# Optimization experiments

Measured on AMD Instinct MI355X. Metric: run time of the kernel, lower is better.

Reference implementation:

```python
import jax, jax.numpy as jnp
import numpy as np

NQ, NT, NA = 10000, 50000, 50000
E_GR, E_LT, E_SIM, E_COMP, E_GEN = 50000, 50000, 80000, 100000, 50000
HID, NH, HC, DOT, NL = 512, 4, 128, 256, 2
NEG_SLOPE = 0.2  # PyG GATv2Conv default negative_slope


def _gatv2(x_src, x_dst, src, dst, Wl, bl, Wr, br, att, bias, n_dst):
    # GATv2: x_j = lin_l(x_src), x_i = lin_r(x_dst); e = att . leaky_relu(x_i + x_j)
    xl = (x_src @ Wl + bl).reshape(-1, NH, HC)   # [Ns,H,C]
    xr = (x_dst @ Wr + br).reshape(-1, NH, HC)   # [Nd,H,C]
    m = jax.nn.leaky_relu(xl[src] + xr[dst], NEG_SLOPE)      # [E,H,C]
    logits = jnp.einsum('ehc,hc->eh', m, att)                # [E,H]
    lmax = jax.lax.stop_gradient(jax.ops.segment_max(logits, dst, num_segments=n_dst))
    lmax = jnp.where(jnp.isfinite(lmax), lmax, 0.0)
    ex = jnp.exp(logits - lmax[dst])
    denom = jax.ops.segment_sum(ex, dst, num_segments=n_dst)
    alpha = ex / (denom[dst] + 1e-16)                        # softmax over incoming edges
    out = jax.ops.segment_sum(xl[src] * alpha[:, :, None], dst, num_segments=n_dst)
    return out.reshape(n_dst, NH * HC) + bias


def _layernorm(x, g, b):
    mu = x.mean(-1, keepdims=True)
    var = ((x - mu) ** 2).mean(-1, keepdims=True)
    return (x - mu) / jnp.sqrt(var + 1e-5) * g + b


def _forward(xq, xt, xa, answer_features,
             qp_W, qp_b, tp_W, tp_b, ap_W, ap_b,
             afp_W1, afp_b1, afp_W2, afp_b2,
             conv_Wl, conv_bl, conv_Wr, conv_br, conv_att, conv_bias,
             qh_W, qh_b, qh_g, qh_beta, rh_W, rh_b, rh_g, rh_beta, score_bias,
             ei_gr, ei_lt, ei_sim, ei_comp, ei_gen):
    hq = xq @ qp_W + qp_b
    ht = xt @ tp_W + tp_b
    ha = xa @ ap_W + ap_b
    # add_self_loops=True only for ('query','similar_to','query')
    loops = jnp.arange(NQ, dtype=ei_sim.dtype)
    sim_src = jnp.concatenate([ei_sim[0], loops])
    sim_dst = jnp.concatenate([ei_sim[1], loops])
    for l in range(NL):
        P = lambda r: (conv_Wl[l, r], conv_bl[l, r], conv_Wr[l, r], conv_br[l, r], conv_att[l, r], conv_bias[l, r])
        o_gr = _gatv2(hq, ht, ei_gr[0], ei_gr[1], *P(0), NT)          # query -> think
        o_rgr = _gatv2(ht, hq, ei_gr[1], ei_gr[0], *P(1), NQ)         # think -> query (rev)
        o_lt = _gatv2(ht, ha, ei_lt[0], ei_lt[1], *P(2), NA)          # think -> answer
        o_rlt = _gatv2(ha, ht, ei_lt[1], ei_lt[0], *P(3), NT)         # answer -> think (rev)
        o_sim = _gatv2(hq, hq, sim_src, sim_dst, *P(4), NQ)           # query -> query
        o_cmp = _gatv2(ht, ht, ei_comp[0], ei_comp[1], *P(5), NT)     # think -> think
        # HeteroConv aggr='mean' across relations per destination type, then relu
        hq = jax.nn.relu((o_rgr + o_sim) / 2.0)
        ht = jax.nn.relu((o_gr + o_rlt + o_cmp) / 3.0)
        ha = jax.nn.relu(o_lt)
    q_emb = hq[ei_gen[0]]
    a_emb = ha[ei_gen[1]]
    t_emb = ht[ei_gen[1]]  # faithful to source: think indexed with answer-side index
    af_emb = jax.nn.relu(answer_features @ afp_W1 + afp_b1) @ afp_W2 + afp_b2
    q = _layernorm(q_emb @ qh_W + qh_b, qh_g, qh_beta)
    r = _layernorm(jnp.concatenate([t_emb, a_emb, af_emb], -1) @ rh_W + rh_b, rh_g, rh_beta)
    return (q * r).sum(-1) / jnp.sqrt(jnp.float32(DOT)) + score_bias


def setup_inputs() -> dict:
    ks = jax.random.split(jax.random.key(0), 40)
    n = lambda j, shape, s=0.05: jax.random.normal(ks[j], shape, jnp.float32) * s
    ri = lambda j, shape, hi: jax.random.randint(ks[j], shape, 0, hi, jnp.int32)
    return dict(
        xq=n(0, (NQ, 384), 1.0), xt=n(1, (NT, 384), 1.0), xa=n(2, (NA, 384), 1.0),
        answer_features=n(3, (E_GEN, 6), 1.0),
        qp_W=n(4, (384, HID)), qp_b=n(5, (HID,)),
        tp_W=n(6, (384, HID)), tp_b=n(7, (HID,)),
        ap_W=n(8, (384, HID)), ap_b=n(9, (HID,)),
        afp_W1=n(10, (6, 64)), afp_b1=n(11, (64,)),
        afp_W2=n(12, (64, HID)), afp_b2=n(13, (HID,)),
        conv_Wl=n(14, (NL, 6, HID, HID)), conv_bl=n(15, (NL, 6, HID)),
        conv_Wr=n(16, (NL, 6, HID, HID)), conv_br=n(17, (NL, 6, HID)),
        conv_att=n(18, (NL, 6, NH, HC)), conv_bias=n(19, (NL, 6, HID)),
        qh_W=n(20, (HID, DOT)), qh_b=n(21, (DOT,)),
        qh_g=jnp.ones((DOT,), jnp.float32), qh_beta=jnp.zeros((DOT,), jnp.float32),
        rh_W=n(22, (HID * 3, DOT)), rh_b=n(23, (DOT,)),
        rh_g=jnp.ones((DOT,), jnp.float32), rh_beta=jnp.zeros((DOT,), jnp.float32),
        score_bias=jnp.zeros((1,), jnp.float32),
        ei_gr=jnp.stack([ri(24, (E_GR,), NQ), ri(25, (E_GR,), NT)]),
        ei_lt=jnp.stack([ri(26, (E_LT,), NT), ri(27, (E_LT,), NA)]),
        ei_sim=ri(28, (2, E_SIM), NQ),
        ei_comp=ri(29, (2, E_COMP), NT),
        ei_gen=jnp.stack([ri(30, (E_GEN,), NQ), ri(31, (E_GEN,), NA)]),
    )


def reference(xq, xt, xa, answer_features,
              qp_W, qp_b, tp_W, tp_b, ap_W, ap_b,
              afp_W1, afp_b1, afp_W2, afp_b2,
              conv_Wl, conv_bl, conv_Wr, conv_br, conv_att, conv_bias,
              qh_W, qh_b, qh_g, qh_beta, rh_W, rh_b, rh_g, rh_beta, score_bias,
              ei_gr, ei_lt, ei_sim, ei_comp, ei_gen):
    return _forward(xq, xt, xa, answer_features,
                    qp_W, qp_b, tp_W, tp_b, ap_W, ap_b,
                    afp_W1, afp_b1, afp_W2, afp_b2,
                    conv_Wl, conv_bl, conv_Wr, conv_br, conv_att, conv_bias,
                    qh_W, qh_b, qh_g, qh_beta, rh_W, rh_b, rh_g, rh_beta, score_bias,
                    ei_gr, ei_lt, ei_sim, ei_comp, ei_gen)
```

## Files before the change

kernel.cpp:

```cpp
#include <hip/hip_runtime.h>
#include <cstdio>
#include <type_traits>

#define NQ 10000
#define NT 50000
#define NA 50000
#define E_GR 50000
#define E_LT 50000
#define E_SIM 80000
#define E_COMP 100000
#define E_GEN 50000
#define NEG_SLOPE 0.2f

#define NDTOT 220000
#define NSTOT 220000
#define ETOT  390000
__device__ __constant__ const int c_degOff[7]  = {0, 50000, 60000, 110000, 120000, 170000, 220000};
__device__ __constant__ const int c_sOff[7]    = {0, 10000, 60000, 110000, 120000, 170000, 220000};
__device__ __constant__ const int c_eOff[7]    = {0, 50000, 100000, 150000, 240000, 340000, 390000};
__device__ __constant__ const int c_nb[6]      = {49, 10, 49, 10, 49, 49};
__device__ __constant__ const int c_nbOff[7]   = {0, 49, 59, 108, 118, 167, 216};
__device__ __constant__ const int c_snb[6]     = {10, 49, 49, 10, 49, 49};
__device__ __constant__ const int c_snbOff[7]  = {0, 10, 59, 108, 118, 167, 216};

typedef unsigned short bf16_t;
typedef unsigned int u32;
typedef __attribute__((ext_vector_type(8))) short short8v;
typedef __attribute__((ext_vector_type(4))) float f32x4;

__device__ __forceinline__ float bf2f(u32 bits) { return __uint_as_float(bits << 16); }
__device__ __forceinline__ u32 f2bf(float f) {
  u32 u = __float_as_uint(f);
  return (u + 0x7FFFu + ((u >> 16) & 1u)) >> 16;
}
__device__ __forceinline__ u32 pack2(float a, float b) { return f2bf(a) | (f2bf(b) << 16); }
__device__ __forceinline__ void unpack8(uint4 u, float* f) {
  f[0] = bf2f(u.x & 0xffffu); f[1] = bf2f(u.x >> 16);
  f[2] = bf2f(u.y & 0xffffu); f[3] = bf2f(u.y >> 16);
  f[4] = bf2f(u.z & 0xffffu); f[5] = bf2f(u.z >> 16);
  f[6] = bf2f(u.w & 0xffffu); f[7] = bf2f(u.w >> 16);
}

__device__ __forceinline__ void gload16(const void* g, void* l) {
  __builtin_amdgcn_global_load_lds(
      (const __attribute__((address_space(1))) void*)g,
      (__attribute__((address_space(3))) void*)l, 16, 0, 0);
}

struct GemmDesc {
  const bf16_t* A; const bf16_t* Bt; const float* bias; void* C;
  const int* ridx; int N; const int* Nc; int K;
};

template <typename CT>
__global__ __launch_bounds__(512, 4) void bgemm(
    GemmDesc d0, GemmDesc d1, GemmDesc d2, GemmDesc d3, int M, int accumulate)
{
  __shared__ short lds[3][12288];
  const int z = blockIdx.z;
  GemmDesc d = (z == 3) ? d3 : (z == 2) ? d2 : (z == 1) ? d1 : d0;
  int N = d.Nc ? *d.Nc : d.N;
  const int K = d.K;

  const int tid = threadIdx.x;
  const int ncol = gridDim.x;
  const int nband = (N + 127) >> 7;
  int lin = blockIdx.y * ncol + blockIdx.x;
  if (lin >= ncol * nband) return;

  int band, col;
  const int full = (nband >> 3) * 8 * ncol;
  if (lin < full) {
    int g = lin >> 3, x = lin & 7;
    band = x + 8 * (g / ncol);
    col  = g % ncol;
  } else {
    int r = lin - full;
    band = (nband & ~7) + r / ncol;
    col  = r % ncol;
  }
  const int bm = band * 128, bn = col * 256;

  const int lane = tid & 63;
  const int w = tid >> 6;
  const int wr = w >> 2, wc = w & 3;
  const int fr = lane & 15, fg = lane >> 4;

  const int kg = (((tid & 3) ^ ((tid >> 3) & 3)) << 3);
  const int rr = tid >> 2;
  int ra = min(bm + rr, N - 1);
  const bf16_t* gA0 = d.A + (size_t)(d.ridx ? d.ridx[ra] : ra) * K + kg;
  const bf16_t* gB0 = d.Bt + (size_t)(bn + rr) * K + kg;
  const bf16_t* gB1 = d.Bt + (size_t)(bn + 128 + rr) * K + kg;
  const int wb = w << 9;

  f32x4 acc[4][4];
#pragma unroll
  for (int i = 0; i < 4; ++i)
#pragma unroll
    for (int j = 0; j < 4; ++j) acc[i][j] = (f32x4){0.f, 0.f, 0.f, 0.f};

  auto stage = [&](int buf, int k0) {
    short* base = &lds[buf][0];
    gload16(gA0 + k0, base + wb);
    gload16(gB0 + k0, base + 4096 + wb);
    gload16(gB1 + k0, base + 8192 + wb);
  };

  const int nsteps = K >> 5;
  stage(0, 0);
  const int co = (fg ^ ((fr >> 1) & 3)) << 3;
  for (int s = 0; s < nsteps; ++s) {
    const int cur = s % 3;
    if (s + 1 < nsteps) {
      stage((s + 1) % 3, (s + 1) << 5);
      asm volatile("s_waitcnt vmcnt(3)" ::: "memory");
    } else {
      asm volatile("s_waitcnt vmcnt(0)" ::: "memory");
    }
    __builtin_amdgcn_s_barrier();
    asm volatile("" ::: "memory");
    const short* LA = &lds[cur][0];
    const short* LB = &lds[cur][4096];
    short8v b[4];
#pragma unroll
    for (int j = 0; j < 4; ++j) {
      int R = wc * 64 + j * 16 + fr;
      b[j] = *(const short8v*)&LB[R * 32 + co];
    }
#pragma unroll
    for (int i = 0; i < 4; ++i) {
      int R = wr * 64 + i * 16 + fr;
      short8v a = *(const short8v*)&LA[R * 32 + co];
#pragma unroll
      for (int j = 0; j < 4; ++j)
        acc[i][j] = __builtin_amdgcn_mfma_f32_16x16x32_bf16(b[j], a,
                                                            acc[i][j], 0, 0, 0);
    }
    asm volatile("" ::: "memory");
  }

  CT* C = (CT*)d.C;
  float4 bv[4];
#pragma unroll
  for (int j = 0; j < 4; ++j) {
    bv[j] = make_float4(0.f, 0.f, 0.f, 0.f);
    if (!accumulate && d.bias)
      bv[j] = *(const float4*)(d.bias + bn + wc * 64 + j * 16 + fg * 4);
  }
#pragma unroll
  for (int i = 0; i < 4; ++i) {
    const int n = bm + wr * 64 + i * 16 + fr;
    if (n >= N) continue;
#pragma unroll
    for (int j = 0; j < 4; ++j) {
      const int m0 = bn + wc * 64 + j * 16 + fg * 4;
      f32x4 v = acc[i][j];
      if constexpr (std::is_same<CT, float>::value) {
        float* p = C + (size_t)n * M + m0;
        if (accumulate) {
          float4 o = *(float4*)p;
          o.x += v[0]; o.y += v[1]; o.z += v[2]; o.w += v[3];
          *(float4*)p = o;
        } else {
          *(float4*)p = make_float4(v[0] + bv[j].x, v[1] + bv[j].y,
                                    v[2] + bv[j].z, v[3] + bv[j].w);
        }
      } else {
        uint2 o;
        o.x = pack2(v[0] + bv[j].x, v[1] + bv[j].y);
        o.y = pack2(v[2] + bv[j].z, v[3] + bv[j].w);
        *(uint2*)(C + (size_t)n * M + m0) = o;
      }
    }
  }
}

__device__ __forceinline__ void wT_tile(
    const float* __restrict__ W, bf16_t* __restrict__ Wt, int K, int M)
{
  __shared__ float sm[32][33];
  int mb = blockIdx.x * 32, kb = blockIdx.y * 32;
  int tx = threadIdx.x & 31, ty = threadIdx.x >> 5;
#pragma unroll
  for (int i = 0; i < 4; ++i)
    sm[ty + i * 8][tx] = W[(size_t)(kb + ty + i * 8) * M + mb + tx];
  __syncthreads();
#pragma unroll
  for (int i = 0; i < 4; ++i)
    Wt[(size_t)(mb + ty + i * 8) * K + kb + tx] = (bf16_t)f2bf(sm[tx][ty + i * 8]);
}

__global__ __launch_bounds__(256) void convert_wT(
    const float* __restrict__ W, bf16_t* __restrict__ Wt, int K, int M)
{
  wT_tile(W + (size_t)blockIdx.z * K * M, Wt + (size_t)blockIdx.z * K * M, K, M);
}
__global__ __launch_bounds__(256) void convert_wT24(
    const float* __restrict__ Wl, bf16_t* __restrict__ wl,
    const float* __restrict__ Wr, bf16_t* __restrict__ wr)
{
  int z = blockIdx.z;
  size_t o = (size_t)(z < 12 ? z : z - 12) * 512 * 512;
  if (z < 12) wT_tile(Wl + o, wl + o, 512, 512);
  else        wT_tile(Wr + o, wr + o, 512, 512);
}
__global__ __launch_bounds__(256) void convert_wT3(
    const float* __restrict__ W0, const float* __restrict__ W1,
    const float* __restrict__ W2, bf16_t* __restrict__ T0,
    bf16_t* __restrict__ T1, bf16_t* __restrict__ T2)
{
  int z = blockIdx.z;
  const float* W = z == 0 ? W0 : z == 1 ? W1 : W2;
  bf16_t* T = z == 0 ? T0 : z == 1 ? T1 : T2;
  wT_tile(W, T, 384, 512);
}
__global__ __launch_bounds__(256) void convert_wT4h(
    const float* __restrict__ qh, const float* __restrict__ rh,
    bf16_t* __restrict__ wqh, bf16_t* __restrict__ wrh)
{
  int z = blockIdx.z;
  if (z == 0) wT_tile(qh, wqh, 512, 256);
  else        wT_tile(rh + (size_t)(z - 1) * 512 * 256,
                      wrh + (size_t)(z - 1) * 256 * 512, 512, 256);
}

__global__ __launch_bounds__(256) void cast_flat(
    const float* __restrict__ in, bf16_t* __restrict__ out, int n4)
{
  int t = blockIdx.x * 256 + threadIdx.x;
  if (t >= n4) return;
  float4 v = ((const float4*)in)[t];
  uint2 o;
  o.x = pack2(v.x, v.y);
  o.y = pack2(v.z, v.w);
  ((uint2*)out)[t] = o;
}

__global__ __launch_bounds__(256) void fold_cvec(
    const float* __restrict__ b2, const float* __restrict__ rh2,
    float* __restrict__ cvec)
{
  int m = threadIdx.x;
  float s = 0.f;
  for (int k = 0; k < 512; ++k) s = fmaf(b2[k], rh2[(size_t)k * 256 + m], s);
  cvec[m] = s;
}

#define N4_XQ (NQ * 96)
#define N4_XT (NT * 96)
#define N4_XA (NA * 96)
__global__ __launch_bounds__(256) void cast3(
    const float* __restrict__ xq, const float* __restrict__ xt,
    const float* __restrict__ xa, bf16_t* __restrict__ xqb,
    bf16_t* __restrict__ xtb, bf16_t* __restrict__ xab)
{
  long g = (long)blockIdx.x * 256 + threadIdx.x;
  const float* in; bf16_t* out; long idx;
  if (g < N4_XQ)                { in = xq; out = xqb; idx = g; }
  else if (g < N4_XQ + N4_XT)   { in = xt; out = xtb; idx = g - N4_XQ; }
  else if (g < N4_XQ + N4_XT + N4_XA) { in = xa; out = xab; idx = g - N4_XQ - N4_XT; }
  else return;
  float4 v = ((const float4*)in)[idx];
  uint2 o;
  o.x = pack2(v.x, v.y);
  o.y = pack2(v.z, v.w);
  ((uint2*)out)[idx] = o;
}

__global__ __launch_bounds__(256) void combine_bias6(
    const float* __restrict__ cb, float* __restrict__ bcAll)
{
  int g = blockIdx.x * 256 + threadIdx.x;
  if (g >= 6 * 512) return;
  int row = g >> 9, j = g & 511;
  int l = row / 3, kind = row % 3;
  const float* b = cb + (size_t)l * 6 * 512;
  float v;
  if (kind == 0)      v = (b[0 * 512 + j] + b[3 * 512 + j] + b[5 * 512 + j]) / 3.f;
  else if (kind == 1) v = (b[1 * 512 + j] + b[4 * 512 + j]) * 0.5f;
  else                v = b[2 * 512 + j];
  bcAll[(size_t)row * 512 + j] = v;
}

__device__ __forceinline__ int find_rel6(int g, const int* off) {
  int r = 0;
#pragma unroll
  for (int k = 1; k < 6; ++k) r += (g >= off[k]);
  return r;
}

__global__ __launch_bounds__(256) void hist6(
    const int* __restrict__ d0, const int* __restrict__ d1,
    const int* __restrict__ d2, const int* __restrict__ d3,
    const int* __restrict__ d4, const int* __restrict__ d5,
    const int* __restrict__ s0p, const int* __restrict__ s1p,
    const int* __restrict__ s2p, const int* __restrict__ s3p,
    const int* __restrict__ s4p, const int* __restrict__ s5p,
    int* __restrict__ degAll, int* __restrict__ sdegAll, int* __restrict__ pos)
{
  int g = blockIdx.x * 256 + threadIdx.x;
  if (g >= ETOT) return;
  int r = find_rel6(g, c_eOff);
  int le = g - c_eOff[r];
  const int* dp = r == 0 ? d0 : r == 1 ? d1 : r == 2 ? d2 : r == 3 ? d3
                : r == 4 ? d4 : d5;
  const int* sp = r == 0 ? s0p : r == 1 ? s1p : r == 2 ? s2p : r == 3 ? s3p
                : r == 4 ? s4p : s5p;
  pos[g] = atomicAdd(&degAll[c_degOff[r] + dp[le]], 1);
  atomicAdd(&sdegAll[c_sOff[r] + sp[le]], 1);
}

__global__ __launch_bounds__(256) void scan1All(
    const int* __restrict__ degAll, const int* __restrict__ sdegAll,
    int* __restrict__ startAll, int* __restrict__ cposAll,
    int* __restrict__ sposAll, int* __restrict__ bsumAll)
{
  __shared__ int sm[256];
  int j = blockIdx.x / 216, bb = blockIdx.x % 216;
  const int* nbOff = (j == 2) ? c_snbOff : c_nbOff;
  const int* dOff  = (j == 2) ? c_sOff : c_degOff;
  const int* in    = (j == 2) ? sdegAll : degAll;
  int* out = j == 0 ? startAll : j == 1 ? cposAll : sposAll;
  int r = 0;
#pragma unroll
  for (int k = 1; k < 6; ++k) r += (bb >= nbOff[k]);
  int lb = bb - nbOff[r];
  int base0 = dOff[r], n = dOff[r + 1] - base0;
  int t = threadIdx.x;
  int base = lb * 1024 + t * 4;
  int v[4], sum = 0;
#pragma unroll
  for (int k = 0; k < 4; ++k) {
    int raw = (base + k < n) ? in[base0 + base + k] : 0;
    v[k] = j == 0 ? raw : j == 1 ? (raw >= 2 ? 1 : 0) : (raw >= 1 ? 1 : 0);
    sum += v[k];
  }
  sm[t] = sum;
  __syncthreads();
  for (int off = 1; off < 256; off <<= 1) {
    int x = (t >= off) ? sm[t - off] : 0;
    __syncthreads();
    sm[t] += x;
    __syncthreads();
  }
  int run = (t > 0) ? sm[t - 1] : 0;
  if (t == 255) bsumAll[j * 384 + r * 64 + lb] = sm[255];
#pragma unroll
  for (int k = 0; k < 4; ++k) {
    if (base + k < n) out[base0 + base + k] = run;
    run += v[k];
  }
}

__global__ __launch_bounds__(64) void scan2All(
    int* __restrict__ bsumAll, int* __restrict__ ccount, int* __restrict__ scount)
{
  __shared__ int sm[64];
  int j = blockIdx.x / 6, r = blockIdx.x % 6;
  int nb = (j == 2) ? c_snb[r] : c_nb[r];
  int t = threadIdx.x;
  int v = (t < nb) ? bsumAll[j * 384 + r * 64 + t] : 0;
  sm[t] = v;
  __syncthreads();
  for (int off = 1; off < 64; off <<= 1) {
    int x = (t >= off) ? sm[t - off] : 0;
    __syncthreads();
    sm[t] += x;
    __syncthreads();
  }
  if (t < nb) bsumAll[j * 384 + r * 64 + t] = sm[t] - v;
  if (t == nb - 1) {
    if (j == 1) ccount[r] = sm[t];
    if (j == 2) scount[r] = sm[t];
  }
}

__global__ __launch_bounds__(256) void scan3All(
    int* __restrict__ startAll, int* __restrict__ cposAll,
    int* __restrict__ sposAll, const int* __restrict__ bsumAll)
{
  int g = blockIdx.x * 256 + threadIdx.x;
  if (g >= 3 * NDTOT) return;
  int j = g / NDTOT, ln0 = g % NDTOT;
  const int* dOff = (j == 2) ? c_sOff : c_degOff;
  int* out = j == 0 ? startAll : j == 1 ? cposAll : sposAll;
  int r = find_rel6(ln0, dOff);
  int ln = ln0 - dOff[r];
  out[ln0] += bsumAll[j * 384 + r * 64 + (ln >> 10)];
}

__global__ __launch_bounds__(256) void scatter6(
    const int* __restrict__ d0, const int* __restrict__ d1,
    const int* __restrict__ d2, const int* __restrict__ d3,
    const int* __restrict__ d4, const int* __restrict__ d5,
    const int* __restrict__ s0p, const int* __restrict__ s1p,
    const int* __restrict__ s2p, const int* __restrict__ s3p,
    const int* __restrict__ s4p, const int* __restrict__ s5p,
    const int* __restrict__ startAll, const int* __restrict__ pos,
    const int* __restrict__ sposAll,
    int* __restrict__ eidxAll, int* __restrict__ srcCAll)
{
  int g = blockIdx.x * 256 + threadIdx.x;
  if (g >= ETOT) return;
  int r = find_rel6(g, c_eOff);
  int le = g - c_eOff[r];
  const int* dp = r == 0 ? d0 : r == 1 ? d1 : r == 2 ? d2 : r == 3 ? d3
                : r == 4 ? d4 : d5;
  const int* sp = r == 0 ? s0p : r == 1 ? s1p : r == 2 ? s2p : r == 3 ? s3p
                : r == 4 ? s4p : s5p;
  eidxAll[c_eOff[r] + startAll[c_degOff[r] + dp[le]] + pos[g]] = le;
  srcCAll[g] = sposAll[c_sOff[r] + sp[le]];
}

__global__ __launch_bounds__(256) void compactBoth(
    const int* __restrict__ degAll, const int* __restrict__ cposAll,
    int* __restrict__ cidxAll,
    const int* __restrict__ sdegAll, const int* __restrict__ sposAll,
    int* __restrict__ sidxAll)
{
  int g = blockIdx.x * 256 + threadIdx.x;
  if (g < NDTOT) {
    if (degAll[g] >= 2) {
      int r = find_rel6(g, c_degOff);
      cidxAll[c_degOff[r] + cposAll[g]] = g - c_degOff[r];
    }
  } else if (g < NDTOT + NSTOT) {
    int h = g - NDTOT;
    if (sdegAll[h] >= 1) {
      int r = find_rel6(h, c_sOff);
      sidxAll[c_sOff[r] + sposAll[h]] = h - c_sOff[r];
    }
  }
}

__global__ __launch_bounds__(256) void gat_fused(
    const bf16_t* __restrict__ xl, const bf16_t* __restrict__ xr,
    const int* __restrict__ srcC, const int* __restrict__ start,
    const int* __restrict__ deg, const int* __restrict__ eidx,
    const int* __restrict__ cpos, const float* __restrict__ att,
    bf16_t* __restrict__ acc, int Nd, int accumulate,
    const float* __restrict__ bc, float inv_div)
{
  int d = blockIdx.x * 4 + (threadIdx.x >> 6);
  if (d >= Nd) return;
  int lane = threadIdx.x & 63;

  float acc8[8] = {0.f, 0.f, 0.f, 0.f, 0.f, 0.f, 0.f, 0.f};
  int n = deg[d], s0 = start[d];
  if (n == 1) {
    int s = srcC[eidx[s0]];
    unpack8(*(const uint4*)(xl + (size_t)s * 512 + lane * 8), acc8);
  } else if (n > 1) {
    float xrr[8];
    unpack8(*(const uint4*)(xr + (size_t)cpos[d] * 512 + lane * 8), xrr);
    float at[8];
    *(float4*)(at)     = *(const float4*)(att + lane * 8);
    *(float4*)(at + 4) = *(const float4*)(att + lane * 8 + 4);
    float den = 0.f;
    int sN = srcC[eidx[s0]];
    for (int i = 0; i < n; ++i) {
      int s = sN;
      if (i + 1 < n) sN = srcC[eidx[s0 + i + 1]];
      float f[8];
      unpack8(*(const uint4*)(xl + (size_t)s * 512 + lane * 8), f);
      float p = 0.f;
#pragma unroll
      for (int k = 0; k < 8; ++k) {
        float x = f[k] + xrr[k];
        p = fmaf(at[k], x >= 0.f ? x : NEG_SLOPE * x, p);
      }
#pragma unroll
      for (int m = 8; m >= 1; m >>= 1) p += __shfl_xor(p, m);
      float ex = __expf(p);
      den += ex;
#pragma unroll
      for (int k = 0; k < 8; ++k) acc8[k] = fmaf(ex, f[k], acc8[k]);
    }
    float inv = 1.f / (den + 1e-16f);
#pragma unroll
    for (int k = 0; k < 8; ++k) acc8[k] *= inv;
  }

  bf16_t* out = acc + (size_t)d * 512 + lane * 8;
  if (accumulate) {
    float old[8];
    unpack8(*(const uint4*)out, old);
#pragma unroll
    for (int k = 0; k < 8; ++k) acc8[k] += old[k];
  }
  if (bc) {
    float bcv[8];
    *(float4*)(bcv)     = *(const float4*)(bc + lane * 8);
    *(float4*)(bcv + 4) = *(const float4*)(bc + lane * 8 + 4);
#pragma unroll
    for (int k = 0; k < 8; ++k)
      acc8[k] = fmaxf(fmaf(acc8[k], inv_div, bcv[k]), 0.f);
  }
  uint4 s;
  s.x = pack2(acc8[0], acc8[1]); s.y = pack2(acc8[2], acc8[3]);
  s.z = pack2(acc8[4], acc8[5]); s.w = pack2(acc8[6], acc8[7]);
  *(uint4*)out = s;
}

__global__ __launch_bounds__(256) void af_hidden(
    const float* __restrict__ af, const float* __restrict__ W1,
    const float* __restrict__ b1, bf16_t* __restrict__ out, int n)
{
  int t = blockIdx.x * blockDim.x + threadIdx.x;
  if (t >= n * 64) return;
  int i = t >> 6, j = t & 63;
  const float* a = af + (size_t)i * 6;
  float s = b1[j];
#pragma unroll
  for (int k = 0; k < 6; ++k) s = fmaf(a[k], W1[k * 64 + j], s);
  out[t] = (bf16_t)f2bf(fmaxf(s, 0.f));
}

__global__ __launch_bounds__(256) void build_sim(
    const int* __restrict__ ei, int* __restrict__ ss, int* __restrict__ sd)
{
  int t = blockIdx.x * blockDim.x + threadIdx.x;
  if (t >= E_SIM + NQ) return;
  if (t < E_SIM) { ss[t] = ei[t]; sd[t] = ei[E_SIM + t]; }
  else           { ss[t] = t - E_SIM; sd[t] = t - E_SIM; }
}

__global__ __launch_bounds__(256) void head_final(
    const float* __restrict__ qn, const float* __restrict__ rn,
    const float* __restrict__ afr, const float* __restrict__ cvec,
    const int* __restrict__ gsrc, const int* __restrict__ gdst,
    const float* __restrict__ qg, const float* __restrict__ qb,
    const float* __restrict__ rg, const float* __restrict__ rb,
    const float* __restrict__ score_bias, float* __restrict__ out, int E)
{
  int e = blockIdx.x * 4 + (threadIdx.x >> 6);
  if (e >= E) return;
  int lane = threadIdx.x & 63;

  float4 q = *(const float4*)(qn + (size_t)gsrc[e] * 256 + lane * 4);
  float s = q.x + q.y + q.z + q.w;
#pragma unroll
  for (int m = 32; m >= 1; m >>= 1) s += __shfl_xor(s, m);
  float mu = s * (1.f / 256.f);
  float dq0 = q.x - mu, dq1 = q.y - mu, dq2 = q.z - mu, dq3 = q.w - mu;
  float v = dq0 * dq0 + dq1 * dq1 + dq2 * dq2 + dq3 * dq3;
#pragma unroll
  for (int m = 32; m >= 1; m >>= 1) v += __shfl_xor(v, m);
  float rstd = rsqrtf(v * (1.f / 256.f) + 1e-5f);
  float4 g4 = *(const float4*)(qg + lane * 4);
  float4 b4 = *(const float4*)(qb + lane * 4);
  float qn0 = dq0 * rstd * g4.x + b4.x, qn1 = dq1 * rstd * g4.y + b4.y;
  float qn2 = dq2 * rstd * g4.z + b4.z, qn3 = dq3 * rstd * g4.w + b4.w;

  float4 r0 = *(const float4*)(rn + (size_t)gdst[e] * 256 + lane * 4);
  float4 r1 = *(const float4*)(afr + (size_t)e * 256 + lane * 4);
  float4 cv = *(const float4*)(cvec + lane * 4);
  float4 r;
  r.x = r0.x + r1.x + cv.x;
  r.y = r0.y + r1.y + cv.y;
  r.z = r0.z + r1.z + cv.z;
  r.w = r0.w + r1.w + cv.w;
  s = r.x + r.y + r.z + r.w;
#pragma unroll
  for (int m = 32; m >= 1; m >>= 1) s += __shfl_xor(s, m);
  mu = s * (1.f / 256.f);
  float dr0 = r.x - mu, dr1 = r.y - mu, dr2 = r.z - mu, dr3 = r.w - mu;
  v = dr0 * dr0 + dr1 * dr1 + dr2 * dr2 + dr3 * dr3;
#pragma unroll
  for (int m = 32; m >= 1; m >>= 1) v += __shfl_xor(v, m);
  rstd = rsqrtf(v * (1.f / 256.f) + 1e-5f);
  g4 = *(const float4*)(rg + lane * 4);
  b4 = *(const float4*)(rb + lane * 4);
  float rn0 = dr0 * rstd * g4.x + b4.x, rn1 = dr1 * rstd * g4.y + b4.y;
  float rn2 = dr2 * rstd * g4.z + b4.z, rn3 = dr3 * rstd * g4.w + b4.w;

  float d = qn0 * rn0 + qn1 * rn1 + qn2 * rn2 + qn3 * rn3;
#pragma unroll
  for (int m = 32; m >= 1; m >>= 1) d += __shfl_xor(d, m);
  if (lane == 0) out[e] = d * 0.0625f + score_bias[0];
}

extern "C" void kernel_launch(void* const* d_in, const int* in_sizes, int n_in,
                              void* d_out, int out_size, void* d_ws, size_t ws_size,
                              hipStream_t stream) {
  (void)in_sizes; (void)n_in; (void)out_size;
  const float* xq      = (const float*)d_in[0];
  const float* xt      = (const float*)d_in[1];
  const float* xa      = (const float*)d_in[2];
  const float* af      = (const float*)d_in[3];
  const float* qp_W    = (const float*)d_in[4];
  const float* qp_b    = (const float*)d_in[5];
  const float* tp_W    = (const float*)d_in[6];
  const float* tp_b    = (const float*)d_in[7];
  const float* ap_W    = (const float*)d_in[8];
  const float* ap_b    = (const float*)d_in[9];
  const float* afp_W1  = (const float*)d_in[10];
  const float* afp_b1  = (const float*)d_in[11];
  const float* afp_W2  = (const float*)d_in[12];
  const float* afp_b2  = (const float*)d_in[13];
  const float* conv_Wl = (const float*)d_in[14];
  const float* conv_bl = (const float*)d_in[15];
  const float* conv_Wr = (const float*)d_in[16];
  const float* conv_br = (const float*)d_in[17];
  const float* conv_att  = (const float*)d_in[18];
  const float* conv_bias = (const float*)d_in[19];
  const float* qh_W    = (const float*)d_in[20];
  const float* qh_b    = (const float*)d_in[21];
  const float* qh_g    = (const float*)d_in[22];
  const float* qh_beta = (const float*)d_in[23];
  const float* rh_W    = (const float*)d_in[24];
  const float* rh_b    = (const float*)d_in[25];
  const float* rh_g    = (const float*)d_in[26];
  const float* rh_beta = (const float*)d_in[27];
  const float* score_b = (const float*)d_in[28];
  const int* ei_gr   = (const int*)d_in[29];
  const int* ei_lt   = (const int*)d_in[30];
  const int* ei_sim  = (const int*)d_in[31];
  const int* ei_comp = (const int*)d_in[32];
  const int* ei_gen  = (const int*)d_in[33];

  char* base = (char*)d_ws;
  size_t off = 0;
  auto alloc = [&](size_t bytes) {
    void* p = base + off;
    off = (off + bytes + 255) & ~(size_t)255;
    return p;
  };
  bf16_t* hq   = (bf16_t*)alloc((size_t)NQ * 512 * 2);
  bf16_t* ht   = (bf16_t*)alloc((size_t)NT * 512 * 2);
  bf16_t* ha   = (bf16_t*)alloc((size_t)NA * 512 * 2);
  bf16_t* acct = (bf16_t*)alloc((size_t)NT * 512 * 2);
  bf16_t* accq = (bf16_t*)alloc((size_t)NQ * 512 * 2);
  bf16_t* arena = (bf16_t*)alloc((size_t)100000 * 512 * 2);
  bf16_t* xlb  = arena;
  bf16_t* xrb  = arena + (size_t)50000 * 512;
  int* simsrc  = (int*)alloc((size_t)(E_SIM + NQ) * 4);
  int* simdst  = (int*)alloc((size_t)(E_SIM + NQ) * 4);

  bf16_t* wqp  = (bf16_t*)alloc((size_t)512 * 384 * 2);
  bf16_t* wtp  = (bf16_t*)alloc((size_t)512 * 384 * 2);
  bf16_t* wap  = (bf16_t*)alloc((size_t)512 * 384 * 2);
  bf16_t* wl   = (bf16_t*)alloc((size_t)12 * 512 * 512 * 2);
  bf16_t* wr   = (bf16_t*)alloc((size_t)12 * 512 * 512 * 2);
  bf16_t* wqh  = (bf16_t*)alloc((size_t)256 * 512 * 2);
  bf16_t* wrh0 = (bf16_t*)alloc((size_t)256 * 512 * 2);
  bf16_t* wrh1 = (bf16_t*)alloc((size_t)256 * 512 * 2);
  bf16_t* wrh2 = (bf16_t*)alloc((size_t)256 * 512 * 2);
  float* bcAll = (float*)alloc(6 * 512 * 4);
  bf16_t* a2b    = (bf16_t*)alloc((size_t)64 * 512 * 2);
  float*  wfoldF = (float*)alloc((size_t)64 * 256 * 4);
  bf16_t* wfoldT = (bf16_t*)alloc((size_t)256 * 64 * 2);
  float*  cvec   = (float*)alloc(256 * 4);

  int* degAll   = (int*)alloc((size_t)NDTOT * 4);
  int* sdegAll  = (int*)alloc((size_t)NSTOT * 4);
  int* startAll = (int*)alloc((size_t)NDTOT * 4);
  int* cposAll  = (int*)alloc((size_t)NDTOT * 4);
  int* cidxAll  = (int*)alloc((size_t)NDTOT * 4);
  int* sposAll  = (int*)alloc((size_t)NSTOT * 4);
  int* sidxAll  = (int*)alloc((size_t)NSTOT * 4);
  int* eidxAll  = (int*)alloc((size_t)ETOT * 4);
  int* srcCAll  = (int*)alloc((size_t)ETOT * 4);
  int* posb     = (int*)alloc((size_t)ETOT * 4);
  int* bsumAll  = (int*)alloc(3 * 6 * 64 * 4);
  int* ccount   = (int*)alloc(6 * 4);
  int* scount   = (int*)alloc(6 * 4);
  if (off > ws_size) {
    fprintf(stderr, "kernel_launch: ws too small, need %zu have %zu\n", off, ws_size);
    return;
  }

  const int degOff[6] = {0, 50000, 60000, 110000, 120000, 170000};
  const int sOff[6]   = {0, 10000, 60000, 110000, 120000, 170000};
  const int eOff[6]   = {0, 50000, 100000, 150000, 240000, 340000};
  auto ROWS = [&](int r) { return arena + (size_t)r * 512; };

  auto mkDesc = [](const bf16_t* A, const bf16_t* Bt, const float* bias, void* C,
                   const int* ridx, int N, const int* Nc, int K) {
    GemmDesc d; d.A = A; d.Bt = Bt; d.bias = bias; d.C = C;
    d.ridx = ridx; d.N = N; d.Nc = Nc; d.K = K; return d;
  };
  GemmDesc dz = mkDesc(nullptr, nullptr, nullptr, nullptr, nullptr, 0, nullptr, 32);

  auto launch_b = [&](GemmDesc a, GemmDesc b, GemmDesc c, GemmDesc d, int nz,
                      int maxN, int M, int acc_) {
    dim3 g(M / 256, (maxN + 127) / 128, nz);
    bgemm<bf16_t><<<g, 512, 0, stream>>>(a, b, c, d, M, acc_);
  };
  auto launch_f = [&](GemmDesc a, GemmDesc b, GemmDesc c, GemmDesc d, int nz,
                      int maxN, int M, int acc_) {
    dim3 g(M / 256, (maxN + 127) / 128, nz);
    bgemm<float><<<g, 512, 0, stream>>>(a, b, c, d, M, acc_);
  };

  convert_wT24<<<dim3(16, 16, 24), 256, 0, stream>>>(conv_Wl, wl, conv_Wr, wr);
  convert_wT3<<<dim3(16, 12, 3), 256, 0, stream>>>(qp_W, tp_W, ap_W, wqp, wtp, wap);
  convert_wT4h<<<dim3(8, 16, 4), 256, 0, stream>>>(qh_W, rh_W, wqh, wrh0);
  combine_bias6<<<(6 * 512 + 255) / 256, 256, 0, stream>>>(conv_bias, bcAll);
  cast_flat<<<(64 * 512 / 4 + 255) / 256, 256, 0, stream>>>(afp_W2, a2b, 64 * 512 / 4);
  launch_f(mkDesc(a2b, wrh2, nullptr, wfoldF, nullptr, 64, nullptr, 512),
           dz, dz, dz, 1, 64, 256, 0);
  convert_wT<<<dim3(8, 2, 1), 256, 0, stream>>>(wfoldF, wfoldT, 64, 256);
  fold_cvec<<<1, 256, 0, stream>>>(afp_b2, rh_W + 1024 * 256, cvec);

  build_sim<<<(E_SIM + NQ + 255) / 256, 256, 0, stream>>>(ei_sim, simsrc, simdst);
  const int* dsts[6]  = {ei_gr + E_GR, ei_gr, ei_lt, simdst,
                         ei_comp + E_COMP, ei_lt + E_LT};
  const int* srcsA[6] = {ei_gr, ei_gr + E_GR, ei_lt + E_LT, simsrc,
                         ei_comp, ei_lt};
  hipMemsetAsync(degAll, 0, (size_t)(sdegAll + NSTOT) - (size_t)degAll, stream);
  hist6<<<(ETOT + 255) / 256, 256, 0, stream>>>(
      dsts[0], dsts[1], dsts[2], dsts[3], dsts[4], dsts[5],
      srcsA[0], srcsA[1], srcsA[2], srcsA[3], srcsA[4], srcsA[5],
      degAll, sdegAll, posb);
  scan1All<<<648, 256, 0, stream>>>(degAll, sdegAll, startAll, cposAll,
                                    sposAll, bsumAll);
  scan2All<<<18, 64, 0, stream>>>(bsumAll, ccount, scount);
  scan3All<<<(3 * NDTOT + 255) / 256, 256, 0, stream>>>(startAll, cposAll,
                                                        sposAll, bsumAll);
  scatter6<<<(ETOT + 255) / 256, 256, 0, stream>>>(
      dsts[0], dsts[1], dsts[2], dsts[3], dsts[4], dsts[5],
      srcsA[0], srcsA[1], srcsA[2], srcsA[3], srcsA[4], srcsA[5],
      startAll, posb, sposAll, eidxAll, srcCAll);
  compactBoth<<<(NDTOT + NSTOT + 255) / 256, 256, 0, stream>>>(
      degAll, cposAll, cidxAll, sdegAll, sposAll, sidxAll);

  cast3<<<((long)(N4_XQ + N4_XT + N4_XA) + 255) / 256, 256, 0, stream>>>(
      xq, xt, xa, accq, xlb, xrb);
  launch_b(mkDesc(accq, wqp, qp_b, hq, nullptr, NQ, nullptr, 384),
           mkDesc(xlb, wtp, tp_b, ht, nullptr, NT, nullptr, 384),
           mkDesc(xrb, wap, ap_b, ha, nullptr, NA, nullptr, 384),
           dz, 3, NT, 512, 0);

  bf16_t *hq_i = hq, *ht_i = ht, *hq_o = accq, *ht_o = acct;
  for (int l = 0; l < 2; ++l) {
    const float* bc_t = bcAll + (size_t)(l * 3 + 0) * 512;
    const float* bc_q = bcAll + (size_t)(l * 3 + 1) * 512;
    const float* bc_a = bcAll + (size_t)(l * 3 + 2) * 512;
    size_t p0 = (size_t)l * 6 + 0;
    size_t p1 = (size_t)l * 6 + 1;
    size_t p3 = (size_t)l * 6 + 3;
    size_t p4 = (size_t)l * 6 + 4;
    size_t p5 = (size_t)l * 6 + 5;
    size_t p2 = (size_t)l * 6 + 2;

    auto gat = [&](int r, const bf16_t* xl_, const bf16_t* xr_, size_t po,
                   bf16_t* acc_, int Nd_, int accum, const float* bc, float inv) {
      gat_fused<<<(Nd_ + 3) / 4, 256, 0, stream>>>(
          xl_, xr_, srcCAll + eOff[r], startAll + degOff[r], degAll + degOff[r],
          eidxAll + eOff[r], cposAll + degOff[r], conv_att + po * 512,
          acc_, Nd_, accum, bc, inv);
    };

    launch_b(mkDesc(hq_i, wl + p0 * 262144, conv_bl + p0 * 512, ROWS(0),
                    sidxAll + sOff[0], 10000, scount + 0, 512),
             mkDesc(ht_i, wr + p0 * 262144, conv_br + p0 * 512, ROWS(10000),
                    cidxAll + degOff[0], 25000, ccount + 0, 512),
             mkDesc(ht_i, wl + p1 * 262144, conv_bl + p1 * 512, ROWS(35000),
                    sidxAll + sOff[1], 50000, scount + 1, 512),
             mkDesc(hq_i, wr + p1 * 262144, conv_br + p1 * 512, ROWS(85000),
                    cidxAll + degOff[1], 10000, ccount + 1, 512),
             4, 50000, 512, 0);
    gat(0, ROWS(0), ROWS(10000), p0, ht_o, NT, 0, nullptr, 0.f);
    gat(1, ROWS(35000), ROWS(85000), p1, hq_o, NQ, 0, nullptr, 0.f);

    launch_b(mkDesc(ha, wl + p3 * 262144, conv_bl + p3 * 512, ROWS(0),
                    sidxAll + sOff[2], 50000, scount + 2, 512),
             mkDesc(ht_i, wr + p3 * 262144, conv_br + p3 * 512, ROWS(50000),
                    cidxAll + degOff[2], 25000, ccount + 2, 512),
             mkDesc(hq_i, wl + p4 * 262144, conv_bl + p4 * 512, ROWS(75000),
                    sidxAll + sOff[3], 10000, scount + 3, 512),
             mkDesc(hq_i, wr + p4 * 262144, conv_br + p4 * 512, ROWS(85000),
                    cidxAll + degOff[3], 10000, ccount + 3, 512),
             4, 50000, 512, 0);
    gat(2, ROWS(0), ROWS(50000), p3, ht_o, NT, 1, nullptr, 0.f);
    gat(3, ROWS(75000), ROWS(85000), p4, hq_o, NQ, 1, bc_q, 0.5f);

    launch_b(mkDesc(ht_i, wl + p5 * 262144, conv_bl + p5 * 512, ROWS(0),
                    sidxAll + sOff[4], 50000, scount + 4, 512),
             mkDesc(ht_i, wr + p5 * 262144, conv_br + p5 * 512, ROWS(50000),
                    cidxAll + degOff[4], 50000, ccount + 4, 512),
             dz, dz, 2, 50000, 512, 0);
    gat(4, ROWS(0), ROWS(50000), p5, ht_o, NT, 1, bc_t, 1.f / 3.f);

    launch_b(mkDesc(ht_i, wl + p2 * 262144, conv_bl + p2 * 512, ROWS(0),
                    sidxAll + sOff[5], 50000, scount + 5, 512),
             mkDesc(ha, wr + p2 * 262144, conv_br + p2 * 512, ROWS(50000),
                    cidxAll + degOff[5], 25000, ccount + 5, 512),
             dz, dz, 2, 50000, 512, 0);
    gat(5, ROWS(0), ROWS(50000), p2, ha, NA, 0, bc_a, 1.f);

    bf16_t* t;
    t = hq_i; hq_i = hq_o; hq_o = t;
    t = ht_i; ht_i = ht_o; ht_o = t;
  }

  float* qn  = (float*)accq;
  float* rn  = (float*)acct;
  float* afr = (float*)xrb;
  bf16_t* afh = xlb;
  const int* gsrc = ei_gen;
  const int* gdst = ei_gen + E_GEN;

  af_hidden<<<(E_GEN * 64 + 255) / 256, 256, 0, stream>>>(af, afp_W1, afp_b1,
                                                          afh, E_GEN);
  launch_f(mkDesc(hq_i, wqh, qh_b, qn, nullptr, NQ, nullptr, 512),
           mkDesc(ht_i, wrh0, rh_b, rn, nullptr, NT, nullptr, 512),
           mkDesc(afh, wfoldT, nullptr, afr, nullptr, E_GEN, nullptr, 64),
           dz, 3, NT, 256, 0);
  launch_f(mkDesc(ha, wrh1, nullptr, rn, nullptr, NA, nullptr, 512),
           dz, dz, dz, 1, NA, 256, 1);
  head_final<<<(E_GEN + 3) / 4, 256, 0, stream>>>(
      qn, rn, afr, cvec, gsrc, gdst,
      qh_g, qh_beta, rh_g, rh_beta, score_b, (float*)d_out, E_GEN);
}
```

Baseline: 1.156 ms.

## Add full-width 128x512 bf16 GEMM kernel so each A row band is loaded once

Adds a new GEMM kernel in which each block computes a 128-row band across all 512 output columns. It stages A once per k-step alongside four B tiles in a 3-stage LDS pipeline, and uses 8x4 MFMA accumulator tiles per wave. Previously the grid split M into two 256-column tiles, so each A band (including gathered rows) was fetched twice. All bf16-output projection GEMMs now use it. The trade-off is more LDS and registers per block (launch bounds drop to 2 blocks per CU), which may lower occupancy and latency hiding.

```diff
diff --git a/kernel.cpp b/kernel.cpp
--- a/kernel.cpp
+++ b/kernel.cpp
@@ -51,6 +51,109 @@
   const bf16_t* A; const bf16_t* Bt; const float* bias; void* C;
   const int* ridx; int N; const int* Nc; int K;
 };
+
+__global__ __launch_bounds__(512, 2) void bgemmW(
+    GemmDesc d0, GemmDesc d1, GemmDesc d2, GemmDesc d3)
+{
+  __shared__ short lds[3][20480];
+  const int z = blockIdx.z;
+  GemmDesc d = (z == 3) ? d3 : (z == 2) ? d2 : (z == 1) ? d1 : d0;
+  int N = d.Nc ? *d.Nc : d.N;
+  const int K = d.K;
+
+  const int tid = threadIdx.x;
+  const int nband = (N + 127) >> 7;
+  int lin = blockIdx.y;
+  if (lin >= nband) return;
+
+  int band;
+  const int full = (nband >> 3) * 8;
+  if (lin < full) { int g = lin >> 3, x = lin & 7; band = x + 8 * g; }
+  else            band = lin;
+  const int bm = band * 128;
+
+  const int lane = tid & 63;
+  const int w = tid >> 6;
+  const int fr = lane & 15, fg = lane >> 4;
+
+  const int kg = (((tid & 3) ^ ((tid >> 3) & 3)) << 3);
+  const int rr = tid >> 2;
+  int ra = min(bm + rr, N - 1);
+  const bf16_t* gA0 = d.A + (size_t)(d.ridx ? d.ridx[ra] : ra) * K + kg;
+  const bf16_t* gB0 = d.Bt + (size_t)(rr)       * K + kg;
+  const bf16_t* gB1 = d.Bt + (size_t)(128 + rr) * K + kg;
+  const bf16_t* gB2 = d.Bt + (size_t)(256 + rr) * K + kg;
+  const bf16_t* gB3 = d.Bt + (size_t)(384 + rr) * K + kg;
+  const int wb = w << 9;
+
+  f32x4 acc[8][4];
+#pragma unroll
+  for (int i = 0; i < 8; ++i)
+#pragma unroll
+    for (int j = 0; j < 4; ++j) acc[i][j] = (f32x4){0.f, 0.f, 0.f, 0.f};
+
+  auto stage = [&](int buf, int k0) {
+    short* base = &lds[buf][0];
+    gload16(gA0 + k0, base + wb);
+    gload16(gB0 + k0, base + 4096 + wb);
+    gload16(gB1 + k0, base + 8192 + wb);
+    gload16(gB2 + k0, base + 12288 + wb);
+    gload16(gB3 + k0, base + 16384 + wb);
+  };
+
+  const int nsteps = K >> 5;
+  stage(0, 0);
+  const int co = (fg ^ ((fr >> 1) & 3)) << 3;
+  for (int s = 0; s < nsteps; ++s) {
+    const int cur = s % 3;
+    if (s + 1 < nsteps) {
+      stage((s + 1) % 3, (s + 1) << 5);
+      asm volatile("s_waitcnt vmcnt(5)" ::: "memory");
+    } else {
+      asm volatile("s_waitcnt vmcnt(0)" ::: "memory");
+    }
+    __builtin_amdgcn_s_barrier();
+    asm volatile("" ::: "memory");
+    const short* LA = &lds[cur][0];
+    const short* LB = &lds[cur][4096];
+    short8v b[4];
+#pragma unroll
+    for (int j = 0; j < 4; ++j) {
+      int R = w * 64 + j * 16 + fr;
+      b[j] = *(const short8v*)&LB[R * 32 + co];
+    }
+#pragma unroll
+    for (int i = 0; i < 8; ++i) {
+      int R = i * 16 + fr;
+      short8v a = *(const short8v*)&LA[R * 32 + co];
+#pragma unroll
+      for (int j = 0; j < 4; ++j)
+        acc[i][j] = __builtin_amdgcn_mfma_f32_16x16x32_bf16(b[j], a,
+                                                            acc[i][j], 0, 0, 0);
+    }
+    asm volatile("" ::: "memory");
+  }
+
+  bf16_t* C = (bf16_t*)d.C;
+  float4 bv[4];
+#pragma unroll
+  for (int j = 0; j < 4; ++j)
+    bv[j] = *(const float4*)(d.bias + w * 64 + j * 16 + fg * 4);
+#pragma unroll
+  for (int i = 0; i < 8; ++i) {
+    const int n = bm + i * 16 + fr;
+    if (n >= N) continue;
+#pragma unroll
+    for (int j = 0; j < 4; ++j) {
+      const int m0 = w * 64 + j * 16 + fg * 4;
+      f32x4 v = acc[i][j];
+      uint2 o;
+      o.x = pack2(v[0] + bv[j].x, v[1] + bv[j].y);
+      o.y = pack2(v[2] + bv[j].z, v[3] + bv[j].w);
+      *(uint2*)(C + (size_t)n * 512 + m0) = o;
+    }
+  }
+}
 
 template <typename CT>
 __global__ __launch_bounds__(512, 4) void bgemm(
@@ -683,10 +786,10 @@
   };
   GemmDesc dz = mkDesc(nullptr, nullptr, nullptr, nullptr, nullptr, 0, nullptr, 32);
 
-  auto launch_b = [&](GemmDesc a, GemmDesc b, GemmDesc c, GemmDesc d, int nz,
-                      int maxN, int M, int acc_) {
-    dim3 g(M / 256, (maxN + 127) / 128, nz);
-    bgemm<bf16_t><<<g, 512, 0, stream>>>(a, b, c, d, M, acc_);
+  auto launch_w = [&](GemmDesc a, GemmDesc b, GemmDesc c, GemmDesc d, int nz,
+                      int maxN) {
+    dim3 g(1, (maxN + 127) / 128, nz);
+    bgemmW<<<g, 512, 0, stream>>>(a, b, c, d);
   };
   auto launch_f = [&](GemmDesc a, GemmDesc b, GemmDesc c, GemmDesc d, int nz,
                       int maxN, int M, int acc_) {
@@ -728,10 +831,10 @@
 
   cast3<<<((long)(N4_XQ + N4_XT + N4_XA) + 255) / 256, 256, 0, stream>>>(
       xq, xt, xa, accq, xlb, xrb);
-  launch_b(mkDesc(accq, wqp, qp_b, hq, nullptr, NQ, nullptr, 384),
+  launch_w(mkDesc(accq, wqp, qp_b, hq, nullptr, NQ, nullptr, 384),
            mkDesc(xlb, wtp, tp_b, ht, nullptr, NT, nullptr, 384),
            mkDesc(xrb, wap, ap_b, ha, nullptr, NA, nullptr, 384),
-           dz, 3, NT, 512, 0);
+           dz, 3, NT);
 
   bf16_t *hq_i = hq, *ht_i = ht, *hq_o = accq, *ht_o = acct;
   for (int l = 0; l < 2; ++l) {
@@ -753,7 +856,7 @@
           acc_, Nd_, accum, bc, inv);
     };
 
-    launch_b(mkDesc(hq_i, wl + p0 * 262144, conv_bl + p0 * 512, ROWS(0),
+    launch_w(mkDesc(hq_i, wl + p0 * 262144, conv_bl + p0 * 512, ROWS(0),
                     sidxAll + sOff[0], 10000, scount + 0, 512),
              mkDesc(ht_i, wr + p0 * 262144, conv_br + p0 * 512, ROWS(10000),
                     cidxAll + degOff[0], 25000, ccount + 0, 512),
@@ -761,11 +864,11 @@
                     sidxAll + sOff[1], 50000, scount + 1, 512),
              mkDesc(hq_i, wr + p1 * 262144, conv_br + p1 * 512, ROWS(85000),
                     cidxAll + degOff[1], 10000, ccount + 1, 512),
-             4, 50000, 512, 0);
+             4, 50000);
     gat(0, ROWS(0), ROWS(10000), p0, ht_o, NT, 0, nullptr, 0.f);
     gat(1, ROWS(35000), ROWS(85000), p1, hq_o, NQ, 0, nullptr, 0.f);
 
-    launch_b(mkDesc(ha, wl + p3 * 262144, conv_bl + p3 * 512, ROWS(0),
+    launch_w(mkDesc(ha, wl + p3 * 262144, conv_bl + p3 * 512, ROWS(0),
                     sidxAll + sOff[2], 50000, scount + 2, 512),
              mkDesc(ht_i, wr + p3 * 262144, conv_br + p3 * 512, ROWS(50000),
                     cidxAll + degOff[2], 25000, ccount + 2, 512),
@@ -773,22 +876,22 @@
                     sidxAll + sOff[3], 10000, scount + 3, 512),
              mkDesc(hq_i, wr + p4 * 262144, conv_br + p4 * 512, ROWS(85000),
                     cidxAll + degOff[3], 10000, ccount + 3, 512),
-             4, 50000, 512, 0);
+             4, 50000);
     gat(2, ROWS(0), ROWS(50000), p3, ht_o, NT, 1, nullptr, 0.f);
     gat(3, ROWS(75000), ROWS(85000), p4, hq_o, NQ, 1, bc_q, 0.5f);
 
-    launch_b(mkDesc(ht_i, wl + p5 * 262144, conv_bl + p5 * 512, ROWS(0),
+    launch_w(mkDesc(ht_i, wl + p5 * 262144, conv_bl + p5 * 512, ROWS(0),
                     sidxAll + sOff[4], 50000, scount + 4, 512),
              mkDesc(ht_i, wr + p5 * 262144, conv_br + p5 * 512, ROWS(50000),
                     cidxAll + degOff[4], 50000, ccount + 4, 512),
-             dz, dz, 2, 50000, 512, 0);
+             dz, dz, 2, 50000);
     gat(4, ROWS(0), ROWS(50000), p5, ht_o, NT, 1, bc_t, 1.f / 3.f);
 
-    launch_b(mkDesc(ht_i, wl + p2 * 262144, conv_bl + p2 * 512, ROWS(0),
+    launch_w(mkDesc(ht_i, wl + p2 * 262144, conv_bl + p2 * 512, ROWS(0),
                     sidxAll + sOff[5], 50000, scount + 5, 512),
              mkDesc(ha, wr + p2 * 262144, conv_br + p2 * 512, ROWS(50000),
                     cidxAll + degOff[5], 25000, ccount + 5, 512),
-             dz, dz, 2, 50000, 512, 0);
+             dz, dz, 2, 50000);
     gat(5, ROWS(0), ROWS(50000), p2, ha, NA, 0, bc_a, 1.f);
 
     bf16_t* t;
```

New measurement: 1.241 ms. 7.3% more time.
